# Performance work log

Measured on AMD Instinct MI355X. Metric: run time of the kernel, lower is better.

The kernel has to match this reference:

```python
import jax, jax.numpy as jnp
import numpy as np
from jax import lax

BITS = 8  # w_p = a_p = 8 (HAWQ int8)

def _round_ste(x):
    # straight-through round (quant-aware training semantics)
    return x + lax.stop_gradient(jnp.round(x) - x)

def _quant_act(x):
    # QuantAct: symmetric per-tensor activation fake-quant; returns (quantized x, scale)
    n = 2.0 ** (BITS - 1) - 1.0
    sf = jnp.maximum(jnp.max(jnp.abs(x)) / n, 1e-8)
    q = jnp.clip(_round_ste(x / sf), -n, n)
    return q * sf, sf

def _quant_conv(x, w, b, pre_sf, stride, pad):
    # QuantConv2d: per-output-channel symmetric weight quant, integer conv on
    # x/pre_sf with rounded weights, rescale by pre_sf * w_sf. Bias quantized at
    # combined scale. Returns (float output, w_sf) for scale propagation.
    n = 2.0 ** (BITS - 1) - 1.0
    w_sf = jnp.maximum(jnp.max(jnp.abs(w), axis=(1, 2, 3)) / n, 1e-8)
    w_int = _round_ste(w / w_sf[:, None, None, None])
    b_sf = w_sf * pre_sf
    b_int = _round_ste(b / b_sf)
    y = lax.conv_general_dilated(x / pre_sf, w_int, (stride, stride),
                                 [(pad, pad), (pad, pad)],
                                 dimension_numbers=('NCHW', 'OIHW', 'NCHW'))
    return (y + b_int[None, :, None, None]) * b_sf[None, :, None, None], w_sf

def _bn(x, g, b, m, v, eps=1e-5):
    # BatchNorm2d in eval mode (running stats), folded into scale/shift
    inv = g / jnp.sqrt(v + eps)
    return x * inv[None, :, None, None] + (b - m * inv)[None, :, None, None]

def _quant_linear(x, w, b, pre_sf):
    # QuantLinear: per-output-row symmetric weight quant
    n = 2.0 ** (BITS - 1) - 1.0
    w_sf = jnp.maximum(jnp.max(jnp.abs(w), axis=1) / n, 1e-8)
    w_int = _round_ste(w / w_sf[:, None])
    b_sf = w_sf * pre_sf
    b_int = _round_ste(b / b_sf)
    return ((x / pre_sf) @ w_int.T + b_int[None, :]) * b_sf[None, :]

def _forward(x, w0, b0, g0, bb0, m0, v0, w1, b1, g1, bb1, m1, v1,
             w2, b2, g2, bb2, m2, v2, w3, b3, g3, bb3, m3, v3,
             w4, b4, g4, bb4, m4, v4, wd, bd):
    x, psf = _quant_act(x)
    x, _ = _quant_conv(x, w0, b0, psf, 1, 1)   # [B,32,32,32]
    x = _bn(x, g0, bb0, m0, v0)
    x, psf = _quant_act(x)
    x, _ = _quant_conv(x, w1, b1, psf, 1, 0)   # 1x1 -> [B,4,32,32]
    x = _bn(x, g1, bb1, m1, v1)
    x, psf = _quant_act(x)
    x, _ = _quant_conv(x, w2, b2, psf, 2, 1)   # [B,32,16,16]
    x = _bn(x, g2, bb2, m2, v2)
    x, psf = _quant_act(x)
    x, _ = _quant_conv(x, w3, b3, psf, 2, 1)   # [B,32,8,8]
    x = _bn(x, g3, bb3, m3, v3)
    x, psf = _quant_act(x)
    x, _ = _quant_conv(x, w4, b4, psf, 1, 1)   # [B,32,8,8]
    x = _bn(x, g4, bb4, m4, v4)
    x, psf = _quant_act(x)
    x = x.reshape(-1, 2048)                    # 32*8*8 = 2048
    x = _quant_linear(x, wd, bd, psf)          # [B,10]
    return jax.nn.softmax(x, axis=0)           # dim=0 as in original module

def setup_inputs() -> dict:
    key = jax.random.key(0)
    ks = jax.random.split(key, 40)
    B = 1024
    inp = {"x": jax.random.normal(ks[0], (B, 3, 32, 32), jnp.float32)}
    conv_shapes = [(32, 3, 3, 3), (4, 32, 1, 1), (32, 4, 3, 3), (32, 32, 3, 3), (32, 32, 3, 3)]
    for i, s in enumerate(conv_shapes):
        c = s[0]
        inp[f"w{i}"] = jax.random.normal(ks[1 + i], s, jnp.float32) * 0.1
        inp[f"b{i}"] = jax.random.normal(ks[6 + i], (c,), jnp.float32) * 0.01
        inp[f"g{i}"] = 1.0 + 0.1 * jax.random.normal(ks[11 + i], (c,), jnp.float32)
        inp[f"bb{i}"] = 0.1 * jax.random.normal(ks[16 + i], (c,), jnp.float32)
        inp[f"m{i}"] = 0.1 * jax.random.normal(ks[21 + i], (c,), jnp.float32)
        inp[f"v{i}"] = 0.5 + jax.random.uniform(ks[26 + i], (c,), jnp.float32)
    inp["wd"] = jax.random.normal(ks[31], (10, 2048), jnp.float32) * 0.05
    inp["bd"] = jnp.zeros((10,), jnp.float32)
    return inp

def reference(x, w0, b0, g0, bb0, m0, v0, w1, b1, g1, bb1, m1, v1,
              w2, b2, g2, bb2, m2, v2, w3, b3, g3, bb3, m3, v3,
              w4, b4, g4, bb4, m4, v4, wd, bd):
    return _forward(x, w0, b0, g0, bb0, m0, v0, w1, b1, g1, bb1, m1, v1,
                    w2, b2, g2, bb2, m2, v2, w3, b3, g3, bb3, m3, v3,
                    w4, b4, g4, bb4, m4, v4, wd, bd)
```

## Files before the change

### kernel.cpp

```cpp
#include <hip/hip_runtime.h>

#define DI __device__ __forceinline__

constexpr int OFF_W0KT = 384;
constexpr int OFF_W0P  = 1248;
constexpr int OFF_W1I  = 2144;
constexpr int OFF_W2KT = 2272;
constexpr int OFF_W3T  = 3424;
constexpr int OFF_W4T  = 13792;
constexpr int OFF_WDI  = 24160;
constexpr int OFF_WSF0 = 44640;
constexpr int OFF_BNS0 = 44672;
constexpr int OFF_BNB0 = 44704;
constexpr int OFF_WSF1 = 44736;
constexpr int OFF_BNS1 = 44740;
constexpr int OFF_BNB1 = 44744;
constexpr int OFF_WSF2 = 44748;
constexpr int OFF_BNS2 = 44780;
constexpr int OFF_BNB2 = 44812;
constexpr int OFF_WSF3 = 44844;
constexpr int OFF_BNS3 = 44876;
constexpr int OFF_BNB3 = 44908;
constexpr int OFF_WSF4 = 44940;
constexpr int OFF_BNS4 = 44972;
constexpr int OFF_BNB4 = 45004;
constexpr int OFF_WSFD = 45036;
constexpr int OFF_LOG  = 45056;
constexpr int OFF_ACT  = 55296;
constexpr long ACT_A_OFF = OFF_ACT;
constexpr long ACT_B_OFF = OFF_ACT + 8388608L;

DI float quantm(float x, float rsf) {
    float q = rintf(x * rsf);
    return fminf(fmaxf(q, -127.0f), 127.0f);
}
DI float get_sf(const unsigned* umax, int slot) {
    const unsigned* p = umax + slot * 64;
    unsigned m = 0u;
    #pragma unroll
    for (int i = 0; i < 64; ++i) m = m > p[i] ? m : p[i];
    return fmaxf(__uint_as_float(m) / 127.0f, 1e-8f);
}
DI void block_max_atomic(float v, unsigned* dst) {
    __shared__ float redm_[4];
    #pragma unroll
    for (int o = 32; o; o >>= 1) v = fmaxf(v, __shfl_down(v, o, 64));
    int wid = threadIdx.x >> 6;
    if ((threadIdx.x & 63) == 0) redm_[wid] = v;
    __syncthreads();
    if (threadIdx.x == 0) {
        int nw = blockDim.x >> 6;
        float m = redm_[0];
        for (int i = 1; i < nw; ++i) m = fmaxf(m, redm_[i]);
        atomicMax(dst + (blockIdx.x & 63), __float_as_uint(m));
    }
}

struct PrepEntry {
    const float *w, *g, *bb, *m, *v;
    float *wsf, *dst, *dst2, *bns, *bnb;
    int K; int has_bn; int mode;
};
struct PrepAll { PrepEntry e[6]; unsigned* umax; };

__global__ __launch_bounds__(256) void k_prep_all(PrepAll pa) {
    int blk = blockIdx.x;
    if (blk == 142) {
        for (int i = threadIdx.x; i < 384; i += 256) pa.umax[i] = 0u;
        return;
    }
    int layer, oc;
    if      (blk < 32)  { layer = 0; oc = blk; }
    else if (blk < 36)  { layer = 1; oc = blk - 32; }
    else if (blk < 68)  { layer = 2; oc = blk - 36; }
    else if (blk < 100) { layer = 3; oc = blk - 68; }
    else if (blk < 132) { layer = 4; oc = blk - 100; }
    else                { layer = 5; oc = blk - 132; }
    PrepEntry a = pa.e[layer];
    const float* wr = a.w + (long)oc * a.K;
    float mx = 0.f;
    for (int i = threadIdx.x; i < a.K; i += 256) mx = fmaxf(mx, fabsf(wr[i]));
    __shared__ float red[4];
    __shared__ float s_sf;
    #pragma unroll
    for (int o = 32; o; o >>= 1) mx = fmaxf(mx, __shfl_down(mx, o, 64));
    if ((threadIdx.x & 63) == 0) red[threadIdx.x >> 6] = mx;
    __syncthreads();
    if (threadIdx.x == 0) {
        float t = fmaxf(fmaxf(red[0], red[1]), fmaxf(red[2], red[3]));
        t = fmaxf(t / 127.0f, 1e-8f);
        a.wsf[oc] = t; s_sf = t;
        if (a.has_bn) {
            float inv = a.g[oc] / sqrtf(a.v[oc] + 1e-5f);
            a.bns[oc] = inv;
            a.bnb[oc] = a.bb[oc] - a.m[oc] * inv;
        }
    }
    __syncthreads();
    float sf = s_sf;
    for (int i = threadIdx.x; i < a.K; i += 256) {
        float q = rintf(wr[i] / sf);
        if (a.mode == 0) {
            a.dst[(long)oc * a.K + i] = q;
        } else if (a.mode == 1) {
            a.dst[i * 32 + oc] = q;
        } else if (a.mode == 2) {
            a.dst[i * 32 + oc] = q;
            a.dst2[oc * 28 + i] = q;
        } else {
            int ph = i / 72, kk = i - ph * 72;
            a.dst[ph * 2592 + kk * 36 + oc] = q;
        }
    }
    if (a.mode == 2 && threadIdx.x == 0) a.dst2[oc * 28 + 27] = 0.f;
}

__global__ __launch_bounds__(256) void k_absmax(const float4* __restrict__ x, int n4, unsigned* dst) {
    float m = 0.f;
    for (int i = blockIdx.x * blockDim.x + threadIdx.x; i < n4; i += gridDim.x * blockDim.x) {
        float4 t = x[i];
        m = fmaxf(m, fmaxf(fmaxf(fabsf(t.x), fabsf(t.y)), fmaxf(fabsf(t.z), fabsf(t.w))));
    }
    block_max_atomic(m, dst);
}

__global__ __launch_bounds__(256) void k_conv0maxN(
    const float* __restrict__ x, const float* __restrict__ w0kt,
    const float* __restrict__ wsf0, const float* __restrict__ bias0,
    const float* __restrict__ bns0, const float* __restrict__ bnb0,
    const unsigned* __restrict__ umax, unsigned* __restrict__ mout) {
    __shared__ float tile[3 * 18 * 36];
    __shared__ float wlds[27 * 32];
    __shared__ float As[32], Cs[32];
    const int b  = blockIdx.x >> 1;
    const int r0 = (blockIdx.x & 1) * 16;
    const int tid = threadIdx.x;
    const float sfx = get_sf(umax, 0);
    const float rsfx = 1.0f / sfx;
    if (tid < 32) {
        int oc = tid;
        float bsf = wsf0[oc] * sfx;
        float bint = rintf(bias0[oc] / bsf);
        float a = bsf * bns0[oc];
        As[oc] = a;
        Cs[oc] = fmaf(bint, a, bnb0[oc]);
    }
    for (int i = tid; i < 1944; i += 256) tile[i] = 0.f;
    if (tid < 216) ((float4*)wlds)[tid] = ((const float4*)w0kt)[tid];
    __syncthreads();
    const float* xb = x + (long)b * 3072;
    for (int i = tid; i < 1728; i += 256) {
        int ci = i / 576, rem = i - ci * 576;
        int rr = rem >> 5, cc = rem & 31;
        int gr = r0 - 1 + rr;
        if ((unsigned)gr < 32u)
            tile[ci * 648 + rr * 36 + cc + 1] = quantm(xb[ci * 1024 + gr * 32 + cc], rsfx);
    }
    __syncthreads();
    const int oc0  = (tid >> 5) * 4;
    const int pxg  = tid & 31;
    const int row  = pxg >> 1;
    const int wcol = (pxg & 1) * 16;
    float acc[4][16];
    #pragma unroll
    for (int o = 0; o < 4; ++o)
        #pragma unroll
        for (int p = 0; p < 16; ++p) acc[o][p] = 0.f;
    #pragma unroll 1
    for (int kk = 0; kk < 9; ++kk) {
        int ci = kk / 3, ky = kk - ci * 3;
        const float* rp = tile + ci * 648 + (row + ky) * 36 + wcol;
        float wn[20];
        #pragma unroll
        for (int d = 0; d < 5; ++d) *(float4*)&wn[4 * d] = *(const float4*)&rp[4 * d];
        #pragma unroll
        for (int kx = 0; kx < 3; ++kx) {
            float4 wv = *(const float4*)&wlds[(kk * 3 + kx) * 32 + oc0];
            const float* wf = &wv.x;
            #pragma unroll
            for (int o = 0; o < 4; ++o)
                #pragma unroll
                for (int p = 0; p < 16; ++p)
                    acc[o][p] = fmaf(wn[p + kx], wf[o], acc[o][p]);
        }
    }
    float lmax = 0.f;
    #pragma unroll
    for (int o = 0; o < 4; ++o) {
        float A = As[oc0 + o], C = Cs[oc0 + o];
        #pragma unroll
        for (int p = 0; p < 16; ++p)
            lmax = fmaxf(lmax, fabsf(fmaf(acc[o][p], A, C)));
    }
    block_max_atomic(lmax, mout);
}

__global__ __launch_bounds__(256) void k_conv01n(
    const float* __restrict__ x, const float* __restrict__ w0p,
    const float* __restrict__ wsf0, const float* __restrict__ bias0,
    const float* __restrict__ bns0, const float* __restrict__ bnb0,
    const float* __restrict__ w1i,
    const float* __restrict__ wsf1, const float* __restrict__ bias1,
    const float* __restrict__ bns1, const float* __restrict__ bnb1,
    const unsigned* __restrict__ umax, unsigned* __restrict__ mout,
    float* __restrict__ out) {
    __shared__ float tile[1944];
    __shared__ float wls0[896];
    __shared__ float wls1[128];
    __shared__ float Aq[32], Cq[32];
    __shared__ float A1s[4], C1s[4];
    const int b  = blockIdx.x >> 1;
    const int r0 = (blockIdx.x & 1) * 16;
    const int tid = threadIdx.x;
    const float sfx = get_sf(umax, 0);
    const float rsfx = 1.0f / sfx;
    const float sf1 = get_sf(umax, 1);
    const float rsf1 = 1.0f / sf1;
    if (tid < 32) {
        int oc = tid;
        float bsf = wsf0[oc] * sfx;
        float bint = rintf(bias0[oc] / bsf);
        float a = bsf * bns0[oc];
        float c = fmaf(bint, a, bnb0[oc]);
        Aq[oc] = a * rsf1;
        Cq[oc] = c * rsf1;
    }
    if (tid >= 64 && tid < 68) {
        int oc = tid - 64;
        float bsf = wsf1[oc] * sf1;
        float bint = rintf(bias1[oc] / bsf);
        float a = bsf * bns1[oc];
        A1s[oc] = a;
        C1s[oc] = fmaf(bint, a, bnb1[oc]);
    }
    for (int i = tid; i < 1944; i += 256) tile[i] = 0.f;
    if (tid < 224) ((float4*)wls0)[tid] = ((const float4*)w0p)[tid];
    if (tid >= 128 && tid < 256) {
        int j = tid - 128;
        wls1[(j & 31) * 4 + (j >> 5)] = w1i[j];
    }
    __syncthreads();
    const float* xb = x + (long)b * 3072;
    for (int i = tid; i < 1728; i += 256) {
        int ci = i / 576, rem = i - ci * 576;
        int rr = rem >> 5, cc = rem & 31;
        int gr = r0 - 1 + rr;
        if ((unsigned)gr < 32u)
            tile[ci * 648 + rr * 36 + cc + 1] = quantm(xb[ci * 1024 + gr * 32 + cc], rsfx);
    }
    __syncthreads();
    const int h   = tid >> 4;
    const int w0c = (tid & 15) * 2;
    float win[3][3][4];
    #pragma unroll
    for (int ci = 0; ci < 3; ++ci)
        #pragma unroll
        for (int ky = 0; ky < 3; ++ky) {
            const int base = ci * 648 + (h + ky) * 36 + w0c;
            #pragma unroll
            for (int d = 0; d < 4; ++d) win[ci][ky][d] = tile[base + d];
        }
    float acc1[4][2];
    #pragma unroll
    for (int o = 0; o < 4; ++o) { acc1[o][0] = 0.f; acc1[o][1] = 0.f; }
    #pragma unroll 1
    for (int oc = 0; oc < 32; ++oc) {
        float wreg[28];
        const float4* wp4 = (const float4*)&wls0[oc * 28];
        #pragma unroll
        for (int d = 0; d < 7; ++d) *(float4*)&wreg[4 * d] = wp4[d];
        float a0 = 0.f, a1 = 0.f;
        #pragma unroll
        for (int ci = 0; ci < 3; ++ci)
            #pragma unroll
            for (int ky = 0; ky < 3; ++ky)
                #pragma unroll
                for (int kx = 0; kx < 3; ++kx) {
                    float wv = wreg[ci * 9 + ky * 3 + kx];
                    a0 = fmaf(win[ci][ky][kx],     wv, a0);
                    a1 = fmaf(win[ci][ky][kx + 1], wv, a1);
                }
        float A = Aq[oc], C = Cq[oc];
        float q0 = fminf(fmaxf(rintf(fmaf(a0, A, C)), -127.0f), 127.0f);
        float q1 = fminf(fmaxf(rintf(fmaf(a1, A, C)), -127.0f), 127.0f);
        const float4 w1v = *(const float4*)&wls1[oc * 4];
        acc1[0][0] = fmaf(q0, w1v.x, acc1[0][0]); acc1[0][1] = fmaf(q1, w1v.x, acc1[0][1]);
        acc1[1][0] = fmaf(q0, w1v.y, acc1[1][0]); acc1[1][1] = fmaf(q1, w1v.y, acc1[1][1]);
        acc1[2][0] = fmaf(q0, w1v.z, acc1[2][0]); acc1[2][1] = fmaf(q1, w1v.z, acc1[2][1]);
        acc1[3][0] = fmaf(q0, w1v.w, acc1[3][0]); acc1[3][1] = fmaf(q1, w1v.w, acc1[3][1]);
    }
    float lmax = 0.f;
    float* ob = out + (long)b * 4096 + (r0 + h) * 32 + w0c;
    #pragma unroll
    for (int o = 0; o < 4; ++o) {
        float y0 = fmaf(acc1[o][0], A1s[o], C1s[o]);
        float y1 = fmaf(acc1[o][1], A1s[o], C1s[o]);
        lmax = fmaxf(lmax, fmaxf(fabsf(y0), fabsf(y1)));
        float2 r2; r2.x = y0; r2.y = y1;
        *(float2*)&ob[o * 1024] = r2;
    }
    block_max_atomic(lmax, mout);
}

__global__ __launch_bounds__(256) void k_conv2c(
    const float* __restrict__ inp, const float* __restrict__ w2kt,
    const float* __restrict__ wsf, const float* __restrict__ bias,
    const float* __restrict__ bns, const float* __restrict__ bnb,
    const unsigned* __restrict__ umax, unsigned* __restrict__ mout,
    float* __restrict__ out) {
    __shared__ float tile[4 * 34 * 36];
    __shared__ float wlds[36 * 32];
    __shared__ float As[32], Cs[32];
    const int tid = threadIdx.x;
    const float sf = get_sf(umax, 2);
    const float rsf = 1.0f / sf;
    if (tid < 32) {
        int oc = tid;
        float bsf = wsf[oc] * sf;
        float bint = rintf(bias[oc] / bsf);
        float a = bsf * bns[oc];
        As[oc] = a;
        Cs[oc] = fmaf(bint, a, bnb[oc]);
    }
    for (int i = tid; i < 4896; i += 256) tile[i] = 0.f;
    for (int i = tid; i < 288; i += 256) ((float4*)wlds)[i] = ((const float4*)w2kt)[i];
    __syncthreads();
    const float* ib = inp + (long)blockIdx.x * 4096;
    for (int i = tid; i < 4096; i += 256) {
        int ci = i >> 10, px = i & 1023;
        int iy = px >> 5, ix = px & 31;
        tile[ci * 1224 + (iy + 1) * 36 + (ix + 1)] = quantm(ib[i], rsf);
    }
    __syncthreads();
    const int oc0 = (tid >> 6) * 8;
    const int pxq = tid & 63;
    const int h = pxq >> 2, c = pxq & 3;
    float acc[8][4];
    #pragma unroll
    for (int k = 0; k < 8; ++k)
        #pragma unroll
        for (int p = 0; p < 4; ++p) acc[k][p] = 0.f;
    #pragma unroll 1
    for (int ci = 0; ci < 4; ++ci) {
        #pragma unroll
        for (int ky = 0; ky < 3; ++ky) {
            const float* rp = tile + ci * 1224 + (2 * h + ky) * 36 + 8 * c;
            float wn[12];
            #pragma unroll
            for (int d = 0; d < 3; ++d) *(float4*)&wn[4 * d] = *(const float4*)&rp[4 * d];
            #pragma unroll
            for (int kx = 0; kx < 3; ++kx) {
                const float* wp = &wlds[(ci * 9 + ky * 3 + kx) * 32 + oc0];
                float4 wa = *(const float4*)&wp[0];
                float4 wb = *(const float4*)&wp[4];
                float wf[8] = {wa.x, wa.y, wa.z, wa.w, wb.x, wb.y, wb.z, wb.w};
                #pragma unroll
                for (int k = 0; k < 8; ++k)
                    #pragma unroll
                    for (int p = 0; p < 4; ++p)
                        acc[k][p] = fmaf(wn[2 * p + kx], wf[k], acc[k][p]);
            }
        }
    }
    float lmax = 0.f;
    float* ob = out + (long)blockIdx.x * 8192;
    #pragma unroll
    for (int k = 0; k < 8; ++k) {
        int oc = oc0 + k;
        float A = As[oc], C = Cs[oc];
        float4 r;
        float* rp = &r.x;
        #pragma unroll
        for (int p = 0; p < 4; ++p) {
            float y = fmaf(acc[k][p], A, C);
            rp[p] = y;
            lmax = fmaxf(lmax, fabsf(y));
        }
        *(float4*)&ob[oc * 256 + h * 16 + c * 4] = r;
    }
    block_max_atomic(lmax, mout);
}

template<int HIN, int S>
__global__ __launch_bounds__(256) void k_conv34c(
    const float* __restrict__ inp, const float* __restrict__ wt,
    const float* __restrict__ wsf, const float* __restrict__ bias,
    const float* __restrict__ bns, const float* __restrict__ bnb,
    const unsigned* __restrict__ umax, int slot, unsigned* __restrict__ mout,
    float* __restrict__ out) {
    constexpr int ROWS = HIN + 2;
    constexpr int RS   = (S == 2) ? 20 : 12;
    constexpr int TI   = 8 * ROWS * RS;
    constexpr int PIX  = HIN * HIN;
    constexpr int NELT = 8 * PIX;
    constexpr int WINW = S + 3;
    __shared__ float tile[TI];
    __shared__ float wlds[72 * 36];
    __shared__ float As[32], Cs[32];
    const int tid = threadIdx.x;
    const int ocg = tid >> 5;
    const int pxq = tid & 31;
    const int h = pxq >> 2, c = pxq & 3;
    const float sf = get_sf(umax, slot);
    const float rsf = 1.0f / sf;
    if (tid < 32) {
        int oc = tid;
        float bsf = wsf[oc] * sf;
        float bint = rintf(bias[oc] / bsf);
        float a = bsf * bns[oc];
        As[oc] = a;
        Cs[oc] = fmaf(bint, a, bnb[oc]);
    }
    for (int i = tid; i < TI; i += 256) tile[i] = 0.f;
    float acc[4][2];
    #pragma unroll
    for (int k = 0; k < 4; ++k) { acc[k][0] = 0.f; acc[k][1] = 0.f; }
    const float* ib = inp + (long)blockIdx.x * 32 * PIX;
    const float4* wt4 = (const float4*)wt;
    for (int ph = 0; ph < 4; ++ph) {
        __syncthreads();
        for (int i = tid; i < NELT; i += 256) {
            int ci = i / PIX;
            int px = i - ci * PIX;
            int iy = px / HIN, ix = px & (HIN - 1);
            tile[ci * (ROWS * RS) + (iy + 1) * RS + (ix + 1)] =
                quantm(ib[(long)(ph * 8 + ci) * PIX + px], rsf);
        }
        for (int i = tid; i < 648; i += 256) ((float4*)wlds)[i] = wt4[ph * 648 + i];
        __syncthreads();
        #pragma unroll 2
        for (int ci = 0; ci < 8; ++ci) {
            float win[3][WINW];
            #pragma unroll
            for (int ky = 0; ky < 3; ++ky) {
                const int base = ci * (ROWS * RS) + (S * h + ky) * RS + S * 2 * c;
                #pragma unroll
                for (int d = 0; d < WINW; ++d) win[ky][d] = tile[base + d];
            }
            #pragma unroll
            for (int ky = 0; ky < 3; ++ky)
                #pragma unroll
                for (int kx = 0; kx < 3; ++kx) {
                    int j = ky * 3 + kx;
                    float4 wv = *(const float4*)&wlds[(ci * 9 + j) * 36 + ocg * 4];
                    float x0 = win[ky][kx], x1 = win[ky][S + kx];
                    acc[0][0] = fmaf(x0, wv.x, acc[0][0]); acc[0][1] = fmaf(x1, wv.x, acc[0][1]);
                    acc[1][0] = fmaf(x0, wv.y, acc[1][0]); acc[1][1] = fmaf(x1, wv.y, acc[1][1]);
                    acc[2][0] = fmaf(x0, wv.z, acc[2][0]); acc[2][1] = fmaf(x1, wv.z, acc[2][1]);
                    acc[3][0] = fmaf(x0, wv.w, acc[3][0]); acc[3][1] = fmaf(x1, wv.w, acc[3][1]);
                }
        }
    }
    float lmax = 0.f;
    #pragma unroll
    for (int k = 0; k < 4; ++k) {
        int oc = ocg * 4 + k;
        float A = As[oc], C = Cs[oc];
        float y0 = fmaf(acc[k][0], A, C);
        float y1 = fmaf(acc[k][1], A, C);
        lmax = fmaxf(lmax, fmaxf(fabsf(y0), fabsf(y1)));
        float2 r2; r2.x = y0; r2.y = y1;
        *(float2*)&out[((long)blockIdx.x * 32 + oc) * 64 + h * 8 + c * 2] = r2;
    }
    block_max_atomic(lmax, mout);
}

__global__ __launch_bounds__(256) void k_fc(
    const float* __restrict__ act, const float* __restrict__ wdi,
    const float* __restrict__ wsfd, const float* __restrict__ bd,
    const unsigned* __restrict__ umax, float* __restrict__ logits) {
    int b = blockIdx.x;
    float sf = get_sf(umax, 5);
    float rsf = 1.0f / sf;
    const float* ab = act + (long)b * 2048;
    float acc[10];
    #pragma unroll
    for (int c = 0; c < 10; ++c) acc[c] = 0.f;
    #pragma unroll
    for (int k = 0; k < 8; ++k) {
        int j = threadIdx.x + 256 * k;
        float q = quantm(ab[j], rsf);
        #pragma unroll
        for (int c = 0; c < 10; ++c) acc[c] = fmaf(q, wdi[c * 2048 + j], acc[c]);
    }
    #pragma unroll
    for (int c = 0; c < 10; ++c)
        #pragma unroll
        for (int o = 32; o; o >>= 1) acc[c] += __shfl_down(acc[c], o, 64);
    __shared__ float red[4][10];
    int wid = threadIdx.x >> 6;
    if ((threadIdx.x & 63) == 0)
        #pragma unroll
        for (int c = 0; c < 10; ++c) red[wid][c] = acc[c];
    __syncthreads();
    if (threadIdx.x < 10) {
        int c = threadIdx.x;
        float s = red[0][c] + red[1][c] + red[2][c] + red[3][c];
        float bsf = wsfd[c] * sf;
        float bint = rintf(bd[c] / bsf);
        logits[b * 10 + c] = (s + bint) * bsf;
    }
}

__global__ __launch_bounds__(256) void k_softmax(const float* __restrict__ logits, float* __restrict__ out) {
    int c = blockIdx.x;
    float v0 = logits[(threadIdx.x +   0) * 10 + c];
    float v1 = logits[(threadIdx.x + 256) * 10 + c];
    float v2 = logits[(threadIdx.x + 512) * 10 + c];
    float v3 = logits[(threadIdx.x + 768) * 10 + c];
    float mx = fmaxf(fmaxf(v0, v1), fmaxf(v2, v3));
    __shared__ float redm[4];
    __shared__ float reds[4];
    #pragma unroll
    for (int o = 32; o; o >>= 1) mx = fmaxf(mx, __shfl_down(mx, o, 64));
    if ((threadIdx.x & 63) == 0) redm[threadIdx.x >> 6] = mx;
    __syncthreads();
    mx = fmaxf(fmaxf(redm[0], redm[1]), fmaxf(redm[2], redm[3]));
    float e0 = expf(v0 - mx), e1 = expf(v1 - mx), e2 = expf(v2 - mx), e3 = expf(v3 - mx);
    float s = (e0 + e1) + (e2 + e3);
    #pragma unroll
    for (int o = 32; o; o >>= 1) s += __shfl_down(s, o, 64);
    if ((threadIdx.x & 63) == 0) reds[threadIdx.x >> 6] = s;
    __syncthreads();
    s = reds[0] + reds[1] + reds[2] + reds[3];
    out[(threadIdx.x +   0) * 10 + c] = e0 / s;
    out[(threadIdx.x + 256) * 10 + c] = e1 / s;
    out[(threadIdx.x + 512) * 10 + c] = e2 / s;
    out[(threadIdx.x + 768) * 10 + c] = e3 / s;
}

extern "C" void kernel_launch(void* const* d_in, const int* in_sizes, int n_in,
                              void* d_out, int out_size, void* d_ws, size_t ws_size,
                              hipStream_t stream) {
    (void)in_sizes; (void)n_in; (void)out_size; (void)ws_size;
    const float* x = (const float*)d_in[0];
    const float *w[5], *bia[5], *g[5], *bb[5], *m[5], *v[5];
    for (int i = 0; i < 5; ++i) {
        w[i]   = (const float*)d_in[1 + 6 * i + 0];
        bia[i] = (const float*)d_in[1 + 6 * i + 1];
        g[i]   = (const float*)d_in[1 + 6 * i + 2];
        bb[i]  = (const float*)d_in[1 + 6 * i + 3];
        m[i]   = (const float*)d_in[1 + 6 * i + 4];
        v[i]   = (const float*)d_in[1 + 6 * i + 5];
    }
    const float* wd = (const float*)d_in[31];
    const float* bd = (const float*)d_in[32];
    float* ws = (float*)d_ws;
    unsigned* umax = (unsigned*)ws;
    float* out = (float*)d_out;

    float* w0kt = ws + OFF_W0KT;
    float* w0p  = ws + OFF_W0P;
    float* w1i  = ws + OFF_W1I;
    float* w2kt = ws + OFF_W2KT;
    float* w3t  = ws + OFF_W3T;
    float* w4t  = ws + OFF_W4T;
    float* wdi  = ws + OFF_WDI;
    float* wsf0 = ws + OFF_WSF0; float* bns0 = ws + OFF_BNS0; float* bnb0 = ws + OFF_BNB0;
    float* wsf1 = ws + OFF_WSF1; float* bns1 = ws + OFF_BNS1; float* bnb1 = ws + OFF_BNB1;
    float* wsf2 = ws + OFF_WSF2; float* bns2 = ws + OFF_BNS2; float* bnb2 = ws + OFF_BNB2;
    float* wsf3 = ws + OFF_WSF3; float* bns3 = ws + OFF_BNS3; float* bnb3 = ws + OFF_BNB3;
    float* wsf4 = ws + OFF_WSF4; float* bns4 = ws + OFF_BNS4; float* bnb4 = ws + OFF_BNB4;
    float* wsfd = ws + OFF_WSFD;
    float* logits = ws + OFF_LOG;
    float* actA = ws + ACT_A_OFF;
    float* actB = ws + ACT_B_OFF;

    PrepAll pa;
    pa.umax = umax;
    const float* ww[6] = {w[0], w[1], w[2], w[3], w[4], wd};
    float* wsfp[6] = {wsf0, wsf1, wsf2, wsf3, wsf4, wsfd};
    float* dstp[6] = {w0kt, w1i, w2kt, w3t, w4t, wdi};
    float* dst2p[6] = {w0p, nullptr, nullptr, nullptr, nullptr, nullptr};
    float* bnsp[6] = {bns0, bns1, bns2, bns3, bns4, nullptr};
    float* bnbp[6] = {bnb0, bnb1, bnb2, bnb3, bnb4, nullptr};
    int Ks[6]   = {27, 32, 36, 288, 288, 2048};
    int modes[6] = {2, 0, 1, 3, 3, 0};
    for (int i = 0; i < 6; ++i) {
        pa.e[i].w = ww[i];
        pa.e[i].g = (i < 5) ? g[i] : nullptr;
        pa.e[i].bb = (i < 5) ? bb[i] : nullptr;
        pa.e[i].m = (i < 5) ? m[i] : nullptr;
        pa.e[i].v = (i < 5) ? v[i] : nullptr;
        pa.e[i].wsf = wsfp[i];
        pa.e[i].dst = dstp[i];
        pa.e[i].dst2 = dst2p[i];
        pa.e[i].bns = bnsp[i];
        pa.e[i].bnb = bnbp[i];
        pa.e[i].K = Ks[i];
        pa.e[i].has_bn = (i < 5) ? 1 : 0;
        pa.e[i].mode = modes[i];
    }

    hipLaunchKernelGGL(k_prep_all, dim3(143), dim3(256), 0, stream, pa);
    hipLaunchKernelGGL(k_absmax, dim3(1024), dim3(256), 0, stream,
                       (const float4*)x, 1024 * 3 * 32 * 32 / 4, umax + 0 * 64);
    hipLaunchKernelGGL(k_conv0maxN, dim3(2048), dim3(256), 0, stream,
                       x, w0kt, wsf0, bia[0], bns0, bnb0, umax, umax + 1 * 64);
    hipLaunchKernelGGL(k_conv01n, dim3(2048), dim3(256), 0, stream,
                       x, w0p, wsf0, bia[0], bns0, bnb0,
                       w1i, wsf1, bia[1], bns1, bnb1, umax, umax + 2 * 64, actB);
    hipLaunchKernelGGL(k_conv2c, dim3(1024), dim3(256), 0, stream,
                       actB, w2kt, wsf2, bia[2], bns2, bnb2, umax, umax + 3 * 64, actA);
    hipLaunchKernelGGL((k_conv34c<16, 2>), dim3(1024), dim3(256), 0, stream,
                       actA, w3t, wsf3, bia[3], bns3, bnb3, umax, 3, umax + 4 * 64, actB);
    hipLaunchKernelGGL((k_conv34c<8, 1>),  dim3(1024), dim3(256), 0, stream,
                       actB, w4t, wsf4, bia[4], bns4, bnb4, umax, 4, umax + 5 * 64, actA);
    hipLaunchKernelGGL(k_fc, dim3(1024), dim3(256), 0, stream, actA, wdi, wsfd, bd, umax, logits);
    hipLaunchKernelGGL(k_softmax, dim3(10), dim3(256), 0, stream, logits, out);
}
```

Before: 176.5 us.

## Process full image per block in fused conv0/conv1 kernel with 4-wide outputs

The fused conv0+1x1 conv kernel now has each block handle a whole 32x32 image instead of half, and each thread computes four adjacent output pixels instead of two. This halves the block count and gives more reuse of each weight register load and of the input window. Tile loads become vectorized float4/float2, and the conv3/4 window loads are vectorized too. In exchange, shared memory per block and register pressure go up, which may lower occupancy.

```diff
diff --git a/kernel.cpp b/kernel.cpp
--- a/kernel.cpp
+++ b/kernel.cpp
@@ -204,13 +204,12 @@
     const float* __restrict__ bns1, const float* __restrict__ bnb1,
     const unsigned* __restrict__ umax, unsigned* __restrict__ mout,
     float* __restrict__ out) {
-    __shared__ float tile[1944];
+    __shared__ float tile[3672];
     __shared__ float wls0[896];
     __shared__ float wls1[128];
     __shared__ float Aq[32], Cq[32];
     __shared__ float A1s[4], C1s[4];
-    const int b  = blockIdx.x >> 1;
-    const int r0 = (blockIdx.x & 1) * 16;
+    const int b   = blockIdx.x;
     const int tid = threadIdx.x;
     const float sfx = get_sf(umax, 0);
     const float rsfx = 1.0f / sfx;
@@ -233,7 +232,7 @@
         A1s[oc] = a;
         C1s[oc] = fmaf(bint, a, bnb1[oc]);
     }
-    for (int i = tid; i < 1944; i += 256) tile[i] = 0.f;
+    for (int i = tid; i < 3672; i += 256) tile[i] = 0.f;
     if (tid < 224) ((float4*)wls0)[tid] = ((const float4*)w0p)[tid];
     if (tid >= 128 && tid < 256) {
         int j = tid - 128;
@@ -241,35 +240,35 @@
     }
     __syncthreads();
     const float* xb = x + (long)b * 3072;
-    for (int i = tid; i < 1728; i += 256) {
-        int ci = i / 576, rem = i - ci * 576;
-        int rr = rem >> 5, cc = rem & 31;
-        int gr = r0 - 1 + rr;
-        if ((unsigned)gr < 32u)
-            tile[ci * 648 + rr * 36 + cc + 1] = quantm(xb[ci * 1024 + gr * 32 + cc], rsfx);
-    }
-    __syncthreads();
-    const int h   = tid >> 4;
-    const int w0c = (tid & 15) * 2;
-    float win[3][3][4];
+    for (int i = tid; i < 3072; i += 256) {
+        int ci = i >> 10, px = i & 1023;
+        int iy = px >> 5, ix = px & 31;
+        tile[ci * 1224 + (iy + 1) * 36 + (ix + 1)] = quantm(xb[i], rsfx);
+    }
+    __syncthreads();
+    const int h   = tid >> 3;
+    const int w0c = (tid & 7) * 4;
+    float win[3][3][6];
     #pragma unroll
     for (int ci = 0; ci < 3; ++ci)
         #pragma unroll
         for (int ky = 0; ky < 3; ++ky) {
-            const int base = ci * 648 + (h + ky) * 36 + w0c;
-            #pragma unroll
-            for (int d = 0; d < 4; ++d) win[ci][ky][d] = tile[base + d];
-        }
-    float acc1[4][2];
-    #pragma unroll
-    for (int o = 0; o < 4; ++o) { acc1[o][0] = 0.f; acc1[o][1] = 0.f; }
+            const int base = ci * 1224 + (h + ky) * 36 + w0c;
+            *(float4*)&win[ci][ky][0] = *(const float4*)&tile[base];
+            *(float2*)&win[ci][ky][4] = *(const float2*)&tile[base + 4];
+        }
+    float acc1[4][4];
+    #pragma unroll
+    for (int o = 0; o < 4; ++o)
+        #pragma unroll
+        for (int p = 0; p < 4; ++p) acc1[o][p] = 0.f;
     #pragma unroll 1
     for (int oc = 0; oc < 32; ++oc) {
         float wreg[28];
         const float4* wp4 = (const float4*)&wls0[oc * 28];
         #pragma unroll
         for (int d = 0; d < 7; ++d) *(float4*)&wreg[4 * d] = wp4[d];
-        float a0 = 0.f, a1 = 0.f;
+        float a0 = 0.f, a1 = 0.f, a2 = 0.f, a3 = 0.f;
         #pragma unroll
         for (int ci = 0; ci < 3; ++ci)
             #pragma unroll
@@ -277,27 +276,37 @@
                 #pragma unroll
                 for (int kx = 0; kx < 3; ++kx) {
                     float wv = wreg[ci * 9 + ky * 3 + kx];
-                    a0 = fmaf(win[ci][ky][kx],     wv, a0);
+                    a0 = fmaf(win[ci][ky][kx + 0], wv, a0);
                     a1 = fmaf(win[ci][ky][kx + 1], wv, a1);
+                    a2 = fmaf(win[ci][ky][kx + 2], wv, a2);
+                    a3 = fmaf(win[ci][ky][kx + 3], wv, a3);
                 }
         float A = Aq[oc], C = Cq[oc];
         float q0 = fminf(fmaxf(rintf(fmaf(a0, A, C)), -127.0f), 127.0f);
         float q1 = fminf(fmaxf(rintf(fmaf(a1, A, C)), -127.0f), 127.0f);
+        float q2 = fminf(fmaxf(rintf(fmaf(a2, A, C)), -127.0f), 127.0f);
+        float q3 = fminf(fmaxf(rintf(fmaf(a3, A, C)), -127.0f), 127.0f);
         const float4 w1v = *(const float4*)&wls1[oc * 4];
         acc1[0][0] = fmaf(q0, w1v.x, acc1[0][0]); acc1[0][1] = fmaf(q1, w1v.x, acc1[0][1]);
+        acc1[0][2] = fmaf(q2, w1v.x, acc1[0][2]); acc1[0][3] = fmaf(q3, w1v.x, acc1[0][3]);
         acc1[1][0] = fmaf(q0, w1v.y, acc1[1][0]); acc1[1][1] = fmaf(q1, w1v.y, acc1[1][1]);
+        acc1[1][2] = fmaf(q2, w1v.y, acc1[1][2]); acc1[1][3] = fmaf(q3, w1v.y, acc1[1][3]);
         acc1[2][0] = fmaf(q0, w1v.z, acc1[2][0]); acc1[2][1] = fmaf(q1, w1v.z, acc1[2][1]);
+        acc1[2][2] = fmaf(q2, w1v.z, acc1[2][2]); acc1[2][3] = fmaf(q3, w1v.z, acc1[2][3]);
         acc1[3][0] = fmaf(q0, w1v.w, acc1[3][0]); acc1[3][1] = fmaf(q1, w1v.w, acc1[3][1]);
+        acc1[3][2] = fmaf(q2, w1v.w, acc1[3][2]); acc1[3][3] = fmaf(q3, w1v.w, acc1[3][3]);
     }
     float lmax = 0.f;
-    float* ob = out + (long)b * 4096 + (r0 + h) * 32 + w0c;
+    float* ob = out + (long)b * 4096 + h * 32 + w0c;
     #pragma unroll
     for (int o = 0; o < 4; ++o) {
         float y0 = fmaf(acc1[o][0], A1s[o], C1s[o]);
         float y1 = fmaf(acc1[o][1], A1s[o], C1s[o]);
-        lmax = fmaxf(lmax, fmaxf(fabsf(y0), fabsf(y1)));
-        float2 r2; r2.x = y0; r2.y = y1;
-        *(float2*)&ob[o * 1024] = r2;
+        float y2 = fmaf(acc1[o][2], A1s[o], C1s[o]);
+        float y3 = fmaf(acc1[o][3], A1s[o], C1s[o]);
+        lmax = fmaxf(lmax, fmaxf(fmaxf(fabsf(y0), fabsf(y1)), fmaxf(fabsf(y2), fabsf(y3))));
+        float4 r4; r4.x = y0; r4.y = y1; r4.z = y2; r4.w = y3;
+        *(float4*)&ob[o * 1024] = r4;
     }
     block_max_atomic(lmax, mout);
 }
@@ -434,8 +443,13 @@
             #pragma unroll
             for (int ky = 0; ky < 3; ++ky) {
                 const int base = ci * (ROWS * RS) + (S * h + ky) * RS + S * 2 * c;
-                #pragma unroll
-                for (int d = 0; d < WINW; ++d) win[ky][d] = tile[base + d];
+                if (S == 2) {
+                    *(float4*)&win[ky][0] = *(const float4*)&tile[base];
+                    win[ky][4] = tile[base + 4];
+                } else {
+                    *(float2*)&win[ky][0] = *(const float2*)&tile[base];
+                    *(float2*)&win[ky][2] = *(const float2*)&tile[base + 2];
+                }
             }
             #pragma unroll
             for (int ky = 0; ky < 3; ++ky)
@@ -597,7 +611,7 @@
                        (const float4*)x, 1024 * 3 * 32 * 32 / 4, umax + 0 * 64);
     hipLaunchKernelGGL(k_conv0maxN, dim3(2048), dim3(256), 0, stream,
                        x, w0kt, wsf0, bia[0], bns0, bnb0, umax, umax + 1 * 64);
-    hipLaunchKernelGGL(k_conv01n, dim3(2048), dim3(256), 0, stream,
+    hipLaunchKernelGGL(k_conv01n, dim3(1024), dim3(256), 0, stream,
                        x, w0p, wsf0, bia[0], bns0, bnb0,
                        w1i, wsf1, bia[1], bns1, bnb1, umax, umax + 2 * 64, actB);
     hipLaunchKernelGGL(k_conv2c, dim3(1024), dim3(256), 0, stream,
```

Result: no change. 176.0 us (-0.3%).
